# Kernel optimization log

Measured on AMD Instinct MI355X. Metric: run time of the kernel, lower is better.

## Reference

```python
import jax, jax.numpy as jnp
import numpy as np

N = 524288            # total ray samples
EMB_DIM = 32          # hash embedder out_dim (16 levels x 2 feats)
DIR_DIM = 27          # freq embedder out_dim (3 + 3*2*4)
GEO_FEAT = 15         # cfg.geo_feature_dim
LATENT_DIM = 128      # cfg.latent_code_dim
NUM_LATENT = 100      # cfg.num_latent_code
D_HIDDEN = 64
RGB_IN = EMB_DIM + DIR_DIM + GEO_FEAT + LATENT_DIM  # 202


def setup_inputs() -> dict:
    key = jax.random.key(0)
    ks = jax.random.split(key, 16)

    def lin(k, fan_in, fan_out):
        # torch nn.Linear default init: U(-1/sqrt(fan_in), 1/sqrt(fan_in))
        bound = 1.0 / np.sqrt(fan_in)
        kw, kb = jax.random.split(k)
        W = jax.random.uniform(kw, (fan_in, fan_out), jnp.float32, -bound, bound)
        b = jax.random.uniform(kb, (fan_out,), jnp.float32, -bound, bound)
        return W, b

    occ_W0, occ_b0 = lin(ks[0], EMB_DIM, D_HIDDEN)
    occ_W1, occ_b1 = lin(ks[1], D_HIDDEN, D_HIDDEN)
    occ_W2, occ_b2 = lin(ks[2], D_HIDDEN, 1 + GEO_FEAT)
    rgb_W0, rgb_b0 = lin(ks[3], RGB_IN, D_HIDDEN)
    rgb_W1, rgb_b1 = lin(ks[4], D_HIDDEN, D_HIDDEN)
    rgb_W2, rgb_b2 = lin(ks[5], D_HIDDEN, 3)

    # kaiming_normal_ init of rgb_latent
    rgb_latent = jax.random.normal(ks[6], (NUM_LATENT, LATENT_DIM), jnp.float32) * np.sqrt(2.0 / LATENT_DIM)

    embedded = jax.random.normal(ks[7], (N, EMB_DIM), jnp.float32)
    embedded_dir = jax.random.normal(ks[8], (N, DIR_DIM), jnp.float32)

    return {
        'embedded': embedded, 'embedded_dir': embedded_dir,
        'occ_W0': occ_W0, 'occ_b0': occ_b0,
        'occ_W1': occ_W1, 'occ_b1': occ_b1,
        'occ_W2': occ_W2, 'occ_b2': occ_b2,
        'rgb_W0': rgb_W0, 'rgb_b0': rgb_b0,
        'rgb_W1': rgb_W1, 'rgb_b1': rgb_b1,
        'rgb_W2': rgb_W2, 'rgb_b2': rgb_b2,
        'rgb_latent': rgb_latent,
        'latent_index': 7,
    }


def reference(embedded, embedded_dir,
              occ_W0, occ_b0, occ_W1, occ_b1, occ_W2, occ_b2,
              rgb_W0, rgb_b0, rgb_W1, rgb_b1, rgb_W2, rgb_b2,
              rgb_latent, latent_index):
    sp = jax.nn.softplus
    # occ MLP: softplus hidden layers, linear output
    h = sp(embedded @ occ_W0 + occ_b0)
    h = sp(h @ occ_W1 + occ_b1)
    hidden = h @ occ_W2 + occ_b2                     # [N, 1+GEO_FEAT]
    occ = 1.0 - jnp.exp(-sp(hidden[:, :1]))          # [N, 1]
    feature = hidden[:, 1:]                          # [N, GEO_FEAT]
    # latent gather: one latent code broadcast over all N samples
    n = embedded.shape[0]
    latent = jnp.broadcast_to(rgb_latent[latent_index], (n, rgb_latent.shape[1]))
    x = jnp.concatenate([embedded, embedded_dir, feature, latent], axis=-1)  # [N, 202]
    # rgb MLP
    r = sp(x @ rgb_W0 + rgb_b0)
    r = sp(r @ rgb_W1 + rgb_b1)
    rgb = jax.nn.sigmoid(r @ rgb_W2 + rgb_b2)        # [N, 3]
    raw = jnp.concatenate([rgb, occ], axis=-1)       # [N, 4]
    return raw, occ
```

## Files before the change

kernel.cpp:

```cpp
#include <hip/hip_runtime.h>

typedef __bf16 bf16x8 __attribute__((ext_vector_type(8)));
typedef float f32x4 __attribute__((ext_vector_type(4)));
typedef unsigned int u32x4 __attribute__((ext_vector_type(4)));
typedef unsigned int u32x2 __attribute__((ext_vector_type(2)));
typedef u32x4 u32x4a __attribute__((may_alias));
typedef u32x2 u32x2a __attribute__((may_alias));
typedef f32x4 f32x4a __attribute__((may_alias));
typedef unsigned int u32a __attribute__((may_alias));

#define NITER 8

__device__ inline unsigned short f2b(float f) {
    unsigned int x;
    __builtin_memcpy(&x, &f, 4);
    unsigned int r = (x + 0x7FFFu + ((x >> 16) & 1u)) >> 16;
    return (unsigned short)r;
}
__device__ inline unsigned int cvt_pk_bf16(float lo, float hi) {
    unsigned int r;
    asm("v_cvt_pk_bf16_f32 %0, %1, %2" : "=v"(r) : "v"(lo), "v"(hi));
    return r;
}
__device__ inline float vexp2(float x) { float r; asm("v_exp_f32 %0, %1" : "=v"(r) : "v"(x)); return r; }
__device__ inline float vlog2(float x) { float r; asm("v_log_f32 %0, %1" : "=v"(r) : "v"(x)); return r; }
__device__ inline float vrcp(float x)  { float r; asm("v_rcp_f32 %0, %1" : "=v"(r) : "v"(x)); return r; }
__device__ inline float softplus_f(float x) {
    return 0.69314718f * vlog2(1.f + vexp2(1.44269504f * x));
}
__device__ inline float sigmoid_f(float x) {
    return vrcp(1.f + vexp2(-1.44269504f * x));
}
__device__ inline bf16x8 as_bf16x8(u32x4 v) { return __builtin_bit_cast(bf16x8, v); }


__global__ __launch_bounds__(256) void prep_weights(
    const float* __restrict__ oW0, const float* __restrict__ ob0,
    const float* __restrict__ oW1, const float* __restrict__ ob1,
    const float* __restrict__ oW2, const float* __restrict__ ob2,
    const float* __restrict__ rW0, const float* __restrict__ rb0,
    const float* __restrict__ rW1, const float* __restrict__ rb1,
    const float* __restrict__ rW2, const float* __restrict__ rb2,
    const float* __restrict__ rlat, const int* __restrict__ lidx,
    float* __restrict__ wsf, ushort* __restrict__ wsw)
{
    const int bid = blockIdx.x, tid = threadIdx.x;
    __shared__ float red[256];

    if (bid == 0) {
        for (int i = tid; i < 224; i += 256) {
            float v;
            if (i < 64)       v = ob0[i];
            else if (i < 128) v = ob1[i - 64];
            else if (i < 144) v = ob2[i - 128];
            else if (i < 208) v = rb1[i - 144];
            else              v = (i - 208 < 3) ? rb2[i - 208] : 0.f;
            wsf[i] = v;
        }
    }
    if (bid == 7) {
        const int outn = tid & 63, sl = tid >> 6;
        const float* lat = rlat + (size_t)lidx[0] * 128;
        float p = 0.f;
        for (int k = sl * 32; k < sl * 32 + 32; k++)
            p = fmaf(lat[k], rW0[(74 + k) * 64 + outn], p);
        red[tid] = p;
        __syncthreads();
        if (tid < 64)
            wsf[224 + tid] = rb0[tid] + red[tid] + red[64 + tid] + red[128 + tid] + red[192 + tid];
    }
    for (int t = tid; t < 288; t += 256) {
        const int s = bid * 288 + t;
        const int frag = s >> 6, lane = s & 63;
        const int qq = lane >> 4, cc = lane & 15;
        const float* W;
        int ldn = 64, nt = 0, kt = 0;
        bool isr0 = false, isr2 = false;
        if (frag < 4)       { W = oW0; nt = frag; kt = 0; }
        else if (frag < 12) { W = oW1; int f = frag - 4;  nt = f >> 1; kt = f & 1; }
        else if (frag < 14) { W = oW2; ldn = 16; nt = 0; kt = frag - 12; }
        else if (frag < 26) { W = rW0; int f = frag - 14; nt = f / 3; kt = f - nt * 3; isr0 = true; }
        else if (frag < 34) { W = rW1; int f = frag - 26; nt = f >> 1; kt = f & 1; }
        else                { W = rW2; ldn = 3; nt = 0; kt = frag - 34; isr2 = true; }
        const int nn = nt * 16 + cc;
        __align__(16) ushort vals[8];
#pragma unroll
        for (int j = 0; j < 8; j++) {
            int k = kt * 32 + qq * 8 + j;
            float v = 0.f;
            if (isr0) {
                int ks = -1;
                if (k < 59) ks = k;
                else if (k >= 65 && k < 80) ks = k - 65 + 59;
                if (ks >= 0) v = W[ks * 64 + nn];
            } else if (isr2) {
                if (nn < 3) v = W[k * 3 + nn];
            } else {
                v = W[k * ldn + nn];
            }
            vals[j] = f2b(v);
        }
        *(u32x4a*)&wsw[s * 8] = *(const u32x4a*)vals;
    }
}

__global__ __launch_bounds__(512, 4) void net_mfma(
    const float* __restrict__ emb, const float* __restrict__ dir,
    const float* __restrict__ wsf, const ushort* __restrict__ wsw,
    float* __restrict__ out, int n)
{
    __shared__ __align__(16) ushort s_w[36 * 64 * 8];
    __shared__ __align__(16) ushort s_h[8][16 * 72];

    const int tid = threadIdx.x;
    for (int i = tid; i < 36 * 64; i += 512)
        *(u32x4a*)&s_w[i * 8] = *(const u32x4a*)(wsw + i * 8);
    __syncthreads();

    const int wave = tid >> 6, lane = tid & 63, q = lane >> 4, c = lane & 15;
    ushort* hw = s_h[wave];
    for (int i = lane; i < 576; i += 64) ((u32a*)hw)[i] = 0u;

    const int q4 = q * 4;
    f32x4 Bv[18];
#pragma unroll
    for (int nt = 0; nt < 4; nt++) {
        Bv[0 + nt]  = *(const f32x4a*)(wsf + 0   + nt * 16 + q4);
        Bv[4 + nt]  = *(const f32x4a*)(wsf + 64  + nt * 16 + q4);
        Bv[9 + nt]  = *(const f32x4a*)(wsf + 224 + nt * 16 + q4);
        Bv[13 + nt] = *(const f32x4a*)(wsf + 144 + nt * 16 + q4);
    }
    Bv[8]  = *(const f32x4a*)(wsf + 128 + q4);
    Bv[17] = *(const f32x4a*)(wsf + 208 + q4);

    const long dlim = (long)n * 27;

    for (int it = 0; it < NITER; ++it) {
        const long p0 = (long)blockIdx.x * 1024 + it * 128 + wave * 16;

        bf16x8 x_emb, x_dir;
        {
            const float* ep = emb + (p0 + c) * 32 + q * 8;
            f32x4 e0 = *(const f32x4a*)ep;
            f32x4 e1 = *(const f32x4a*)(ep + 4);
            u32x4 pk = {cvt_pk_bf16(e0[0], e0[1]), cvt_pk_bf16(e0[2], e0[3]),
                        cvt_pk_bf16(e1[0], e1[1]), cvt_pk_bf16(e1[2], e1[3])};
            x_emb = as_bf16x8(pk);
        }
        {
            const long ib = (p0 + c) * 27 + q * 8;
            f32x4 d0, d1;
            if (ib + 8 <= dlim) {
                d0 = *(const f32x4a*)(dir + ib);
                d1 = *(const f32x4a*)(dir + ib + 4);
            } else {
#pragma unroll
                for (int j = 0; j < 4; j++) d0[j] = (ib + j < dlim) ? dir[ib + j] : 0.f;
#pragma unroll
                for (int j = 0; j < 4; j++) d1[j] = (ib + 4 + j < dlim) ? dir[ib + 4 + j] : 0.f;
            }
            u32x4 pk = {cvt_pk_bf16(d0[0], d0[1]), cvt_pk_bf16(d0[2], d0[3]),
                        cvt_pk_bf16(d1[0], d1[1]), cvt_pk_bf16(d1[2], d1[3])};
            x_dir = as_bf16x8(pk);
        }

#pragma unroll
        for (int nt = 0; nt < 4; ++nt) {
            f32x4 acc = Bv[0 + nt];
            acc = __builtin_amdgcn_mfma_f32_16x16x32_bf16(
                as_bf16x8(*(const u32x4a*)&s_w[((0 + nt) * 64 + lane) * 8]), x_emb, acc, 0, 0, 0);
            u32x2 pk = {cvt_pk_bf16(softplus_f(acc[0]), softplus_f(acc[1])),
                        cvt_pk_bf16(softplus_f(acc[2]), softplus_f(acc[3]))};
            *(u32x2a*)&hw[c * 72 + nt * 16 + q4] = pk;
        }
        {
            bf16x8 h0 = as_bf16x8(*(const u32x4a*)&hw[c * 72 + 0 + q * 8]);
            bf16x8 h1 = as_bf16x8(*(const u32x4a*)&hw[c * 72 + 32 + q * 8]);
#pragma unroll
            for (int nt = 0; nt < 4; ++nt) {
                f32x4 acc = Bv[4 + nt];
                acc = __builtin_amdgcn_mfma_f32_16x16x32_bf16(
                    as_bf16x8(*(const u32x4a*)&s_w[((4 + nt * 2 + 0) * 64 + lane) * 8]), h0, acc, 0, 0, 0);
                acc = __builtin_amdgcn_mfma_f32_16x16x32_bf16(
                    as_bf16x8(*(const u32x4a*)&s_w[((4 + nt * 2 + 1) * 64 + lane) * 8]), h1, acc, 0, 0, 0);
                u32x2 pk = {cvt_pk_bf16(softplus_f(acc[0]), softplus_f(acc[1])),
                            cvt_pk_bf16(softplus_f(acc[2]), softplus_f(acc[3]))};
                *(u32x2a*)&hw[c * 72 + nt * 16 + q4] = pk;
            }
        }
        float occv;
        {
            bf16x8 h0 = as_bf16x8(*(const u32x4a*)&hw[c * 72 + 0 + q * 8]);
            bf16x8 h1 = as_bf16x8(*(const u32x4a*)&hw[c * 72 + 32 + q * 8]);
            f32x4 acc = Bv[8];
            acc = __builtin_amdgcn_mfma_f32_16x16x32_bf16(
                as_bf16x8(*(const u32x4a*)&s_w[(12 * 64 + lane) * 8]), h0, acc, 0, 0, 0);
            acc = __builtin_amdgcn_mfma_f32_16x16x32_bf16(
                as_bf16x8(*(const u32x4a*)&s_w[(13 * 64 + lane) * 8]), h1, acc, 0, 0, 0);
            occv = sigmoid_f(acc[0]);
            u32x2 pk = {cvt_pk_bf16(acc[0], acc[1]), cvt_pk_bf16(acc[2], acc[3])};
            *(u32x2a*)&hw[c * 72 + q4] = pk;
        }
        {
            bf16x8 x_feat = as_bf16x8(*(const u32x4a*)&hw[c * 72 + q * 8]);
#pragma unroll
            for (int nt = 0; nt < 4; ++nt) {
                f32x4 acc = Bv[9 + nt];
                acc = __builtin_amdgcn_mfma_f32_16x16x32_bf16(
                    as_bf16x8(*(const u32x4a*)&s_w[((14 + nt * 3 + 0) * 64 + lane) * 8]), x_emb, acc, 0, 0, 0);
                acc = __builtin_amdgcn_mfma_f32_16x16x32_bf16(
                    as_bf16x8(*(const u32x4a*)&s_w[((14 + nt * 3 + 1) * 64 + lane) * 8]), x_dir, acc, 0, 0, 0);
                acc = __builtin_amdgcn_mfma_f32_16x16x32_bf16(
                    as_bf16x8(*(const u32x4a*)&s_w[((14 + nt * 3 + 2) * 64 + lane) * 8]), x_feat, acc, 0, 0, 0);
                u32x2 pk = {cvt_pk_bf16(softplus_f(acc[0]), softplus_f(acc[1])),
                            cvt_pk_bf16(softplus_f(acc[2]), softplus_f(acc[3]))};
                *(u32x2a*)&hw[c * 72 + nt * 16 + q4] = pk;
            }
        }
        {
            bf16x8 h0 = as_bf16x8(*(const u32x4a*)&hw[c * 72 + 0 + q * 8]);
            bf16x8 h1 = as_bf16x8(*(const u32x4a*)&hw[c * 72 + 32 + q * 8]);
#pragma unroll
            for (int nt = 0; nt < 4; ++nt) {
                f32x4 acc = Bv[13 + nt];
                acc = __builtin_amdgcn_mfma_f32_16x16x32_bf16(
                    as_bf16x8(*(const u32x4a*)&s_w[((26 + nt * 2 + 0) * 64 + lane) * 8]), h0, acc, 0, 0, 0);
                acc = __builtin_amdgcn_mfma_f32_16x16x32_bf16(
                    as_bf16x8(*(const u32x4a*)&s_w[((26 + nt * 2 + 1) * 64 + lane) * 8]), h1, acc, 0, 0, 0);
                u32x2 pk = {cvt_pk_bf16(softplus_f(acc[0]), softplus_f(acc[1])),
                            cvt_pk_bf16(softplus_f(acc[2]), softplus_f(acc[3]))};
                *(u32x2a*)&hw[c * 72 + nt * 16 + q4] = pk;
            }
        }
        {
            bf16x8 h0 = as_bf16x8(*(const u32x4a*)&hw[c * 72 + 0 + q * 8]);
            bf16x8 h1 = as_bf16x8(*(const u32x4a*)&hw[c * 72 + 32 + q * 8]);
            f32x4 acc = Bv[17];
            acc = __builtin_amdgcn_mfma_f32_16x16x32_bf16(
                as_bf16x8(*(const u32x4a*)&s_w[(34 * 64 + lane) * 8]), h0, acc, 0, 0, 0);
            acc = __builtin_amdgcn_mfma_f32_16x16x32_bf16(
                as_bf16x8(*(const u32x4a*)&s_w[(35 * 64 + lane) * 8]), h1, acc, 0, 0, 0);
            if (q == 0) {
                f32x4 o;
                o[0] = sigmoid_f(acc[0]);
                o[1] = sigmoid_f(acc[1]);
                o[2] = sigmoid_f(acc[2]);
                o[3] = occv;
                *(f32x4a*)&out[(p0 + c) * 4] = o;
                out[(long)4 * n + p0 + c] = occv;
            }
        }
    }
}

extern "C" void kernel_launch(void* const* d_in, const int* in_sizes, int n_in,
                              void* d_out, int out_size, void* d_ws, size_t ws_size,
                              hipStream_t stream) {
    const int n = in_sizes[0] / 32;
    float*  wsf = (float*)d_ws;
    ushort* wsw = (ushort*)((char*)d_ws + 1152);
    prep_weights<<<8, 256, 0, stream>>>(
        (const float*)d_in[2], (const float*)d_in[3],
        (const float*)d_in[4], (const float*)d_in[5],
        (const float*)d_in[6], (const float*)d_in[7],
        (const float*)d_in[8], (const float*)d_in[9],
        (const float*)d_in[10], (const float*)d_in[11],
        (const float*)d_in[12], (const float*)d_in[13],
        (const float*)d_in[14], (const int*)d_in[15],
        wsf, wsw);
    net_mfma<<<n / 1024, 512, 0, stream>>>(
        (const float*)d_in[0], (const float*)d_in[1],
        wsf, wsw, (float*)d_out, n);
}
```

Measured before the change: 195.3 us.

## Process two 16-row tiles per wave to reuse weight fragments across MFMAs

Each wave now handles 32 samples as two 16-row tiles, loading each weight fragment from LDS once and issuing two independent MFMA chains, which halves weight LDS traffic per sample and gives the matrix unit interleaved independent work. Blocks shrink to 256 threads with a padded activation stride of 88, and the launch bound becomes (256, 2). Softplus and sigmoid switch from raw exp/log asm to a numerically stable __expf/__logf form, and the feature packing uses software round-to-nearest-even. The cost is higher register pressure and a lower occupancy hint, plus extra ALU work in the activation functions.

```diff
diff --git a/kernel.cpp b/kernel.cpp
--- a/kernel.cpp
+++ b/kernel.cpp
@@ -10,6 +10,7 @@
 typedef unsigned int u32a __attribute__((may_alias));
 
 #define NITER 8
+#define STR 88
 
 __device__ inline unsigned short f2b(float f) {
     unsigned int x;
@@ -17,19 +18,19 @@
     unsigned int r = (x + 0x7FFFu + ((x >> 16) & 1u)) >> 16;
     return (unsigned short)r;
 }
+__device__ inline unsigned int pack_rne(float a, float b) {
+    return (unsigned int)f2b(a) | ((unsigned int)f2b(b) << 16);
+}
 __device__ inline unsigned int cvt_pk_bf16(float lo, float hi) {
     unsigned int r;
     asm("v_cvt_pk_bf16_f32 %0, %1, %2" : "=v"(r) : "v"(lo), "v"(hi));
     return r;
 }
-__device__ inline float vexp2(float x) { float r; asm("v_exp_f32 %0, %1" : "=v"(r) : "v"(x)); return r; }
-__device__ inline float vlog2(float x) { float r; asm("v_log_f32 %0, %1" : "=v"(r) : "v"(x)); return r; }
-__device__ inline float vrcp(float x)  { float r; asm("v_rcp_f32 %0, %1" : "=v"(r) : "v"(x)); return r; }
 __device__ inline float softplus_f(float x) {
-    return 0.69314718f * vlog2(1.f + vexp2(1.44269504f * x));
+    return fmaxf(x, 0.f) + __logf(1.f + __expf(-fabsf(x)));
 }
 __device__ inline float sigmoid_f(float x) {
-    return vrcp(1.f + vexp2(-1.44269504f * x));
+    return 1.f / (1.f + __expf(-x));
 }
 __device__ inline bf16x8 as_bf16x8(u32x4 v) { return __builtin_bit_cast(bf16x8, v); }
 
@@ -104,24 +105,26 @@
     }
 }
 
-__global__ __launch_bounds__(512, 4) void net_mfma(
+__global__ __launch_bounds__(256, 2) void net_mfma(
     const float* __restrict__ emb, const float* __restrict__ dir,
     const float* __restrict__ wsf, const ushort* __restrict__ wsw,
     float* __restrict__ out, int n)
 {
     __shared__ __align__(16) ushort s_w[36 * 64 * 8];
-    __shared__ __align__(16) ushort s_h[8][16 * 72];
+    __shared__ __align__(16) ushort s_h[4][32 * STR];
 
     const int tid = threadIdx.x;
-    for (int i = tid; i < 36 * 64; i += 512)
+    for (int i = tid; i < 36 * 64; i += 256)
         *(u32x4a*)&s_w[i * 8] = *(const u32x4a*)(wsw + i * 8);
     __syncthreads();
 
     const int wave = tid >> 6, lane = tid & 63, q = lane >> 4, c = lane & 15;
+    const int q4 = q * 4;
     ushort* hw = s_h[wave];
-    for (int i = lane; i < 576; i += 64) ((u32a*)hw)[i] = 0u;
-
-    const int q4 = q * 4;
+    for (int i = lane; i < 32 * STR / 2; i += 64) ((u32a*)hw)[i] = 0u;
+
+    const int rowA = c * STR, rowB = (16 + c) * STR;
+
     f32x4 Bv[18];
 #pragma unroll
     for (int nt = 0; nt < 4; nt++) {
@@ -136,118 +139,150 @@
     const long dlim = (long)n * 27;
 
     for (int it = 0; it < NITER; ++it) {
-        const long p0 = (long)blockIdx.x * 1024 + it * 128 + wave * 16;
-
-        bf16x8 x_emb, x_dir;
-        {
-            const float* ep = emb + (p0 + c) * 32 + q * 8;
-            f32x4 e0 = *(const f32x4a*)ep;
-            f32x4 e1 = *(const f32x4a*)(ep + 4);
-            u32x4 pk = {cvt_pk_bf16(e0[0], e0[1]), cvt_pk_bf16(e0[2], e0[3]),
-                        cvt_pk_bf16(e1[0], e1[1]), cvt_pk_bf16(e1[2], e1[3])};
-            x_emb = as_bf16x8(pk);
-        }
-        {
-            const long ib = (p0 + c) * 27 + q * 8;
-            f32x4 d0, d1;
-            if (ib + 8 <= dlim) {
-                d0 = *(const f32x4a*)(dir + ib);
-                d1 = *(const f32x4a*)(dir + ib + 4);
-            } else {
-#pragma unroll
-                for (int j = 0; j < 4; j++) d0[j] = (ib + j < dlim) ? dir[ib + j] : 0.f;
-#pragma unroll
-                for (int j = 0; j < 4; j++) d1[j] = (ib + 4 + j < dlim) ? dir[ib + 4 + j] : 0.f;
-            }
-            u32x4 pk = {cvt_pk_bf16(d0[0], d0[1]), cvt_pk_bf16(d0[2], d0[3]),
-                        cvt_pk_bf16(d1[0], d1[1]), cvt_pk_bf16(d1[2], d1[3])};
-            x_dir = as_bf16x8(pk);
+        const long p0 = (long)blockIdx.x * 1024 + it * 128 + wave * 32;
+        const long ptA = p0 + c, ptB = p0 + 16 + c;
+
+        bf16x8 xe[2], xd[2];
+#pragma unroll
+        for (int t = 0; t < 2; t++) {
+            const long pt = t ? ptB : ptA;
+            {
+                const float* ep = emb + pt * 32 + q * 8;
+                f32x4 e0 = *(const f32x4a*)ep;
+                f32x4 e1 = *(const f32x4a*)(ep + 4);
+                u32x4 pk = {cvt_pk_bf16(e0[0], e0[1]), cvt_pk_bf16(e0[2], e0[3]),
+                            cvt_pk_bf16(e1[0], e1[1]), cvt_pk_bf16(e1[2], e1[3])};
+                xe[t] = as_bf16x8(pk);
+            }
+            {
+                const long ib = pt * 27 + q * 8;
+                f32x4 d0, d1;
+                if (ib + 8 <= dlim) {
+                    d0 = *(const f32x4a*)(dir + ib);
+                    d1 = *(const f32x4a*)(dir + ib + 4);
+                } else {
+#pragma unroll
+                    for (int j = 0; j < 4; j++) d0[j] = (ib + j < dlim) ? dir[ib + j] : 0.f;
+#pragma unroll
+                    for (int j = 0; j < 4; j++) d1[j] = (ib + 4 + j < dlim) ? dir[ib + 4 + j] : 0.f;
+                }
+                u32x4 pk = {cvt_pk_bf16(d0[0], d0[1]), cvt_pk_bf16(d0[2], d0[3]),
+                            cvt_pk_bf16(d1[0], d1[1]), cvt_pk_bf16(d1[2], d1[3])};
+                xd[t] = as_bf16x8(pk);
+            }
         }
 
 #pragma unroll
         for (int nt = 0; nt < 4; ++nt) {
-            f32x4 acc = Bv[0 + nt];
-            acc = __builtin_amdgcn_mfma_f32_16x16x32_bf16(
-                as_bf16x8(*(const u32x4a*)&s_w[((0 + nt) * 64 + lane) * 8]), x_emb, acc, 0, 0, 0);
-            u32x2 pk = {cvt_pk_bf16(softplus_f(acc[0]), softplus_f(acc[1])),
-                        cvt_pk_bf16(softplus_f(acc[2]), softplus_f(acc[3]))};
-            *(u32x2a*)&hw[c * 72 + nt * 16 + q4] = pk;
-        }
-        {
-            bf16x8 h0 = as_bf16x8(*(const u32x4a*)&hw[c * 72 + 0 + q * 8]);
-            bf16x8 h1 = as_bf16x8(*(const u32x4a*)&hw[c * 72 + 32 + q * 8]);
+            bf16x8 w = as_bf16x8(*(const u32x4a*)&s_w[((0 + nt) * 64 + lane) * 8]);
+            f32x4 aA = __builtin_amdgcn_mfma_f32_16x16x32_bf16(w, xe[0], Bv[0 + nt], 0, 0, 0);
+            f32x4 aB = __builtin_amdgcn_mfma_f32_16x16x32_bf16(w, xe[1], Bv[0 + nt], 0, 0, 0);
+            *(u32x2a*)&hw[rowA + nt * 16 + q4] = u32x2{
+                cvt_pk_bf16(softplus_f(aA[0]), softplus_f(aA[1])),
+                cvt_pk_bf16(softplus_f(aA[2]), softplus_f(aA[3]))};
+            *(u32x2a*)&hw[rowB + nt * 16 + q4] = u32x2{
+                cvt_pk_bf16(softplus_f(aB[0]), softplus_f(aB[1])),
+                cvt_pk_bf16(softplus_f(aB[2]), softplus_f(aB[3]))};
+        }
+        {
+            bf16x8 h0A = as_bf16x8(*(const u32x4a*)&hw[rowA + 0 + q * 8]);
+            bf16x8 h1A = as_bf16x8(*(const u32x4a*)&hw[rowA + 32 + q * 8]);
+            bf16x8 h0B = as_bf16x8(*(const u32x4a*)&hw[rowB + 0 + q * 8]);
+            bf16x8 h1B = as_bf16x8(*(const u32x4a*)&hw[rowB + 32 + q * 8]);
 #pragma unroll
             for (int nt = 0; nt < 4; ++nt) {
-                f32x4 acc = Bv[4 + nt];
-                acc = __builtin_amdgcn_mfma_f32_16x16x32_bf16(
-                    as_bf16x8(*(const u32x4a*)&s_w[((4 + nt * 2 + 0) * 64 + lane) * 8]), h0, acc, 0, 0, 0);
-                acc = __builtin_amdgcn_mfma_f32_16x16x32_bf16(
-                    as_bf16x8(*(const u32x4a*)&s_w[((4 + nt * 2 + 1) * 64 + lane) * 8]), h1, acc, 0, 0, 0);
-                u32x2 pk = {cvt_pk_bf16(softplus_f(acc[0]), softplus_f(acc[1])),
-                            cvt_pk_bf16(softplus_f(acc[2]), softplus_f(acc[3]))};
-                *(u32x2a*)&hw[c * 72 + nt * 16 + q4] = pk;
-            }
-        }
-        float occv;
-        {
-            bf16x8 h0 = as_bf16x8(*(const u32x4a*)&hw[c * 72 + 0 + q * 8]);
-            bf16x8 h1 = as_bf16x8(*(const u32x4a*)&hw[c * 72 + 32 + q * 8]);
-            f32x4 acc = Bv[8];
-            acc = __builtin_amdgcn_mfma_f32_16x16x32_bf16(
-                as_bf16x8(*(const u32x4a*)&s_w[(12 * 64 + lane) * 8]), h0, acc, 0, 0, 0);
-            acc = __builtin_amdgcn_mfma_f32_16x16x32_bf16(
-                as_bf16x8(*(const u32x4a*)&s_w[(13 * 64 + lane) * 8]), h1, acc, 0, 0, 0);
-            occv = sigmoid_f(acc[0]);
-            u32x2 pk = {cvt_pk_bf16(acc[0], acc[1]), cvt_pk_bf16(acc[2], acc[3])};
-            *(u32x2a*)&hw[c * 72 + q4] = pk;
-        }
-        {
-            bf16x8 x_feat = as_bf16x8(*(const u32x4a*)&hw[c * 72 + q * 8]);
+                bf16x8 w0 = as_bf16x8(*(const u32x4a*)&s_w[((4 + nt * 2 + 0) * 64 + lane) * 8]);
+                bf16x8 w1 = as_bf16x8(*(const u32x4a*)&s_w[((4 + nt * 2 + 1) * 64 + lane) * 8]);
+                f32x4 aA = __builtin_amdgcn_mfma_f32_16x16x32_bf16(w0, h0A, Bv[4 + nt], 0, 0, 0);
+                aA = __builtin_amdgcn_mfma_f32_16x16x32_bf16(w1, h1A, aA, 0, 0, 0);
+                f32x4 aB = __builtin_amdgcn_mfma_f32_16x16x32_bf16(w0, h0B, Bv[4 + nt], 0, 0, 0);
+                aB = __builtin_amdgcn_mfma_f32_16x16x32_bf16(w1, h1B, aB, 0, 0, 0);
+                *(u32x2a*)&hw[rowA + nt * 16 + q4] = u32x2{
+                    cvt_pk_bf16(softplus_f(aA[0]), softplus_f(aA[1])),
+                    cvt_pk_bf16(softplus_f(aA[2]), softplus_f(aA[3]))};
+                *(u32x2a*)&hw[rowB + nt * 16 + q4] = u32x2{
+                    cvt_pk_bf16(softplus_f(aB[0]), softplus_f(aB[1])),
+                    cvt_pk_bf16(softplus_f(aB[2]), softplus_f(aB[3]))};
+            }
+        }
+        float occA, occB;
+        {
+            bf16x8 h0A = as_bf16x8(*(const u32x4a*)&hw[rowA + 0 + q * 8]);
+            bf16x8 h1A = as_bf16x8(*(const u32x4a*)&hw[rowA + 32 + q * 8]);
+            bf16x8 h0B = as_bf16x8(*(const u32x4a*)&hw[rowB + 0 + q * 8]);
+            bf16x8 h1B = as_bf16x8(*(const u32x4a*)&hw[rowB + 32 + q * 8]);
+            bf16x8 w0 = as_bf16x8(*(const u32x4a*)&s_w[(12 * 64 + lane) * 8]);
+            bf16x8 w1 = as_bf16x8(*(const u32x4a*)&s_w[(13 * 64 + lane) * 8]);
+            f32x4 aA = __builtin_amdgcn_mfma_f32_16x16x32_bf16(w0, h0A, Bv[8], 0, 0, 0);
+            aA = __builtin_amdgcn_mfma_f32_16x16x32_bf16(w1, h1A, aA, 0, 0, 0);
+            f32x4 aB = __builtin_amdgcn_mfma_f32_16x16x32_bf16(w0, h0B, Bv[8], 0, 0, 0);
+            aB = __builtin_amdgcn_mfma_f32_16x16x32_bf16(w1, h1B, aB, 0, 0, 0);
+            occA = sigmoid_f(aA[0]);
+            occB = sigmoid_f(aB[0]);
+            *(u32x2a*)&hw[rowA + q4] = u32x2{pack_rne(aA[0], aA[1]), pack_rne(aA[2], aA[3])};
+            *(u32x2a*)&hw[rowB + q4] = u32x2{pack_rne(aB[0], aB[1]), pack_rne(aB[2], aB[3])};
+        }
+        {
+            bf16x8 xfA = as_bf16x8(*(const u32x4a*)&hw[rowA + q * 8]);
+            bf16x8 xfB = as_bf16x8(*(const u32x4a*)&hw[rowB + q * 8]);
 #pragma unroll
             for (int nt = 0; nt < 4; ++nt) {
-                f32x4 acc = Bv[9 + nt];
-                acc = __builtin_amdgcn_mfma_f32_16x16x32_bf16(
-                    as_bf16x8(*(const u32x4a*)&s_w[((14 + nt * 3 + 0) * 64 + lane) * 8]), x_emb, acc, 0, 0, 0);
-                acc = __builtin_amdgcn_mfma_f32_16x16x32_bf16(
-                    as_bf16x8(*(const u32x4a*)&s_w[((14 + nt * 3 + 1) * 64 + lane) * 8]), x_dir, acc, 0, 0, 0);
-                acc = __builtin_amdgcn_mfma_f32_16x16x32_bf16(
-                    as_bf16x8(*(const u32x4a*)&s_w[((14 + nt * 3 + 2) * 64 + lane) * 8]), x_feat, acc, 0, 0, 0);
-                u32x2 pk = {cvt_pk_bf16(softplus_f(acc[0]), softplus_f(acc[1])),
-                            cvt_pk_bf16(softplus_f(acc[2]), softplus_f(acc[3]))};
-                *(u32x2a*)&hw[c * 72 + nt * 16 + q4] = pk;
-            }
-        }
-        {
-            bf16x8 h0 = as_bf16x8(*(const u32x4a*)&hw[c * 72 + 0 + q * 8]);
-            bf16x8 h1 = as_bf16x8(*(const u32x4a*)&hw[c * 72 + 32 + q * 8]);
+                bf16x8 w0 = as_bf16x8(*(const u32x4a*)&s_w[((14 + nt * 3 + 0) * 64 + lane) * 8]);
+                bf16x8 w1 = as_bf16x8(*(const u32x4a*)&s_w[((14 + nt * 3 + 1) * 64 + lane) * 8]);
+                bf16x8 w2 = as_bf16x8(*(const u32x4a*)&s_w[((14 + nt * 3 + 2) * 64 + lane) * 8]);
+                f32x4 aA = __builtin_amdgcn_mfma_f32_16x16x32_bf16(w0, xe[0], Bv[9 + nt], 0, 0, 0);
+                aA = __builtin_amdgcn_mfma_f32_16x16x32_bf16(w1, xd[0], aA, 0, 0, 0);
+                aA = __builtin_amdgcn_mfma_f32_16x16x32_bf16(w2, xfA, aA, 0, 0, 0);
+                f32x4 aB = __builtin_amdgcn_mfma_f32_16x16x32_bf16(w0, xe[1], Bv[9 + nt], 0, 0, 0);
+                aB = __builtin_amdgcn_mfma_f32_16x16x32_bf16(w1, xd[1], aB, 0, 0, 0);
+                aB = __builtin_amdgcn_mfma_f32_16x16x32_bf16(w2, xfB, aB, 0, 0, 0);
+                *(u32x2a*)&hw[rowA + nt * 16 + q4] = u32x2{
+                    cvt_pk_bf16(softplus_f(aA[0]), softplus_f(aA[1])),
+                    cvt_pk_bf16(softplus_f(aA[2]), softplus_f(aA[3]))};
+                *(u32x2a*)&hw[rowB + nt * 16 + q4] = u32x2{
+                    cvt_pk_bf16(softplus_f(aB[0]), softplus_f(aB[1])),
+                    cvt_pk_bf16(softplus_f(aB[2]), softplus_f(aB[3]))};
+            }
+        }
+        {
+            bf16x8 h0A = as_bf16x8(*(const u32x4a*)&hw[rowA + 0 + q * 8]);
+            bf16x8 h1A = as_bf16x8(*(const u32x4a*)&hw[rowA + 32 + q * 8]);
+            bf16x8 h0B = as_bf16x8(*(const u32x4a*)&hw[rowB + 0 + q * 8]);
+            bf16x8 h1B = as_bf16x8(*(const u32x4a*)&hw[rowB + 32 + q * 8]);
 #pragma unroll
             for (int nt = 0; nt < 4; ++nt) {
-                f32x4 acc = Bv[13 + nt];
-                acc = __builtin_amdgcn_mfma_f32_16x16x32_bf16(
-                    as_bf16x8(*(const u32x4a*)&s_w[((26 + nt * 2 + 0) * 64 + lane) * 8]), h0, acc, 0, 0, 0);
-                acc = __builtin_amdgcn_mfma_f32_16x16x32_bf16(
-                    as_bf16x8(*(const u32x4a*)&s_w[((26 + nt * 2 + 1) * 64 + lane) * 8]), h1, acc, 0, 0, 0);
-                u32x2 pk = {cvt_pk_bf16(softplus_f(acc[0]), softplus_f(acc[1])),
-                            cvt_pk_bf16(softplus_f(acc[2]), softplus_f(acc[3]))};
-                *(u32x2a*)&hw[c * 72 + nt * 16 + q4] = pk;
-            }
-        }
-        {
-            bf16x8 h0 = as_bf16x8(*(const u32x4a*)&hw[c * 72 + 0 + q * 8]);
-            bf16x8 h1 = as_bf16x8(*(const u32x4a*)&hw[c * 72 + 32 + q * 8]);
-            f32x4 acc = Bv[17];
-            acc = __builtin_amdgcn_mfma_f32_16x16x32_bf16(
-                as_bf16x8(*(const u32x4a*)&s_w[(34 * 64 + lane) * 8]), h0, acc, 0, 0, 0);
-            acc = __builtin_amdgcn_mfma_f32_16x16x32_bf16(
-                as_bf16x8(*(const u32x4a*)&s_w[(35 * 64 + lane) * 8]), h1, acc, 0, 0, 0);
+                bf16x8 w0 = as_bf16x8(*(const u32x4a*)&s_w[((26 + nt * 2 + 0) * 64 + lane) * 8]);
+                bf16x8 w1 = as_bf16x8(*(const u32x4a*)&s_w[((26 + nt * 2 + 1) * 64 + lane) * 8]);
+                f32x4 aA = __builtin_amdgcn_mfma_f32_16x16x32_bf16(w0, h0A, Bv[13 + nt], 0, 0, 0);
+                aA = __builtin_amdgcn_mfma_f32_16x16x32_bf16(w1, h1A, aA, 0, 0, 0);
+                f32x4 aB = __builtin_amdgcn_mfma_f32_16x16x32_bf16(w0, h0B, Bv[13 + nt], 0, 0, 0);
+                aB = __builtin_amdgcn_mfma_f32_16x16x32_bf16(w1, h1B, aB, 0, 0, 0);
+                *(u32x2a*)&hw[rowA + nt * 16 + q4] = u32x2{
+                    cvt_pk_bf16(softplus_f(aA[0]), softplus_f(aA[1])),
+                    cvt_pk_bf16(softplus_f(aA[2]), softplus_f(aA[3]))};
+                *(u32x2a*)&hw[rowB + nt * 16 + q4] = u32x2{
+                    cvt_pk_bf16(softplus_f(aB[0]), softplus_f(aB[1])),
+                    cvt_pk_bf16(softplus_f(aB[2]), softplus_f(aB[3]))};
+            }
+        }
+        {
+            bf16x8 h0A = as_bf16x8(*(const u32x4a*)&hw[rowA + 0 + q * 8]);
+            bf16x8 h1A = as_bf16x8(*(const u32x4a*)&hw[rowA + 32 + q * 8]);
+            bf16x8 h0B = as_bf16x8(*(const u32x4a*)&hw[rowB + 0 + q * 8]);
+            bf16x8 h1B = as_bf16x8(*(const u32x4a*)&hw[rowB + 32 + q * 8]);
+            bf16x8 w0 = as_bf16x8(*(const u32x4a*)&s_w[(34 * 64 + lane) * 8]);
+            bf16x8 w1 = as_bf16x8(*(const u32x4a*)&s_w[(35 * 64 + lane) * 8]);
+            f32x4 aA = __builtin_amdgcn_mfma_f32_16x16x32_bf16(w0, h0A, Bv[17], 0, 0, 0);
+            aA = __builtin_amdgcn_mfma_f32_16x16x32_bf16(w1, h1A, aA, 0, 0, 0);
+            f32x4 aB = __builtin_amdgcn_mfma_f32_16x16x32_bf16(w0, h0B, Bv[17], 0, 0, 0);
+            aB = __builtin_amdgcn_mfma_f32_16x16x32_bf16(w1, h1B, aB, 0, 0, 0);
             if (q == 0) {
-                f32x4 o;
-                o[0] = sigmoid_f(acc[0]);
-                o[1] = sigmoid_f(acc[1]);
-                o[2] = sigmoid_f(acc[2]);
-                o[3] = occv;
-                *(f32x4a*)&out[(p0 + c) * 4] = o;
-                out[(long)4 * n + p0 + c] = occv;
+                f32x4 oA = {sigmoid_f(aA[0]), sigmoid_f(aA[1]), sigmoid_f(aA[2]), occA};
+                f32x4 oB = {sigmoid_f(aB[0]), sigmoid_f(aB[1]), sigmoid_f(aB[2]), occB};
+                *(f32x4a*)&out[ptA * 4] = oA;
+                *(f32x4a*)&out[ptB * 4] = oB;
+                out[(long)4 * n + ptA] = occA;
+                out[(long)4 * n + ptB] = occB;
             }
         }
     }
@@ -268,7 +303,7 @@
         (const float*)d_in[12], (const float*)d_in[13],
         (const float*)d_in[14], (const int*)d_in[15],
         wsf, wsw);
-    net_mfma<<<n / 1024, 512, 0, stream>>>(
+    net_mfma<<<n / 1024, 256, 0, stream>>>(
         (const float*)d_in[0], (const float*)d_in[1],
         wsf, wsw, (float*)d_out, n);
 }
```

After: 251.2 us. 1.29x slower.
